# Performance work log

Hardware: AMD Instinct MI355X
Metric: run time of the kernel (lower is better)

## Reference

```python
import jax, jax.numpy as jnp
import numpy as np

DIM = 512
CODEBOOK_SIZE = 8192


def setup_inputs() -> dict:
    key = jax.random.key(0)
    k_x, k_e = jax.random.split(key)
    x = jax.random.normal(k_x, (4, 4096, DIM), dtype=jnp.float32)
    # EuclideanCodebook buffer: embed ~ randn(codebook_size, dim)
    embed = jax.random.normal(k_e, (CODEBOOK_SIZE, DIM), dtype=jnp.float32)
    return {"x": x, "embed": embed}


def reference(x, embed):
    # projection_in / projection_out are Identity (codebook_dim=None)
    shape = x.shape
    flatten = x.reshape(-1, shape[-1])  # [N, D]
    # dist = -(||f||^2 - 2 f @ e^T + ||e||^2)  -> negative squared euclidean
    f_sq = jnp.sum(flatten * flatten, axis=1, keepdims=True)          # [N, 1]
    e_sq = jnp.sum(embed * embed, axis=1)[None, :]                    # [1, K]
    dist = -(f_sq - 2.0 * flatten @ embed.T + e_sq)                   # [N, K]
    embed_ind = jnp.argmax(dist, axis=-1)                             # [N]
    embed_ind = embed_ind.reshape(shape[:-1])                         # [B, S]
    quantize = jnp.take(embed, embed_ind, axis=0)                     # [B, S, D]
    return quantize, embed_ind
```

## Files before the change

kernel.cpp:

```cpp
#include <hip/hip_runtime.h>

#define DIM    512
#define KCODES 8192
#define NROWS  16384
#define NEG_INF -3.402823466e38f
#define MARGIN 1.0f
#define CPR 128

typedef unsigned short ushort_t;
typedef unsigned int uint_t;
typedef __attribute__((ext_vector_type(8))) short v8s;
typedef __attribute__((ext_vector_type(4))) float v4f;

__device__ inline ushort_t f32_to_bf16_rne(float f) {
    uint_t u = __float_as_uint(f);
    uint_t r = u + 0x7fffu + ((u >> 16) & 1u);
    return (ushort_t)(r >> 16);
}

__device__ inline int4 cvt8hi(float4 a, float4 b) {
    ushort_t h[8] = { f32_to_bf16_rne(a.x), f32_to_bf16_rne(a.y),
                      f32_to_bf16_rne(a.z), f32_to_bf16_rne(a.w),
                      f32_to_bf16_rne(b.x), f32_to_bf16_rne(b.y),
                      f32_to_bf16_rne(b.z), f32_to_bf16_rne(b.w) };
    int4 p;
    p.x = (int)((uint_t)h[0] | ((uint_t)h[1] << 16));
    p.y = (int)((uint_t)h[2] | ((uint_t)h[3] << 16));
    p.z = (int)((uint_t)h[4] | ((uint_t)h[5] << 16));
    p.w = (int)((uint_t)h[6] | ((uint_t)h[7] << 16));
    return p;
}

__device__ inline void dma16(const void* g, void* l) {
    __builtin_amdgcn_global_load_lds(
        (const __attribute__((address_space(1))) unsigned int*)g,
        (__attribute__((address_space(3))) unsigned int*)l, 16, 0, 0);
}

__global__ __launch_bounds__(256) void convert_kernel(
    const float* __restrict__ x, const float* __restrict__ embed,
    int4* __restrict__ e_t, int4* __restrict__ x_t,
    float* __restrict__ e_sq, float* __restrict__ esqh,
    float* __restrict__ f_sq)
{
    __shared__ int4 buf[64][65];

    const int w = threadIdx.x >> 6;
    const int lane = threadIdx.x & 63;
    const bool isE = blockIdx.x < (KCODES / 64);
    const int rows0 = isE ? blockIdx.x * 64 : (blockIdx.x - KCODES / 64) * 64;
    const float* src_base = isE ? embed : x;

    #pragma unroll
    for (int rr = 0; rr < 16; ++rr) {
        int r_local = w * 16 + rr;
        const float* src = src_base + (size_t)(rows0 + r_local) * DIM + lane * 8;
        float4 a = *(const float4*)src;
        float4 b = *(const float4*)(src + 4);
        buf[r_local][(lane + 2 * r_local) & 63] = cvt8hi(a, b);
        float s = a.x*a.x + a.y*a.y + a.z*a.z + a.w*a.w
                + b.x*b.x + b.y*b.y + b.z*b.z + b.w*b.w;
        #pragma unroll
        for (int off = 32; off >= 1; off >>= 1) s += __shfl_down(s, off, 64);
        if (lane == 0) {
            int r = rows0 + r_local;
            if (isE) { e_sq[r] = s; esqh[r] = -0.5f * s; }
            else     { f_sq[r] = s; }
        }
    }
    __syncthreads();

    #pragma unroll
    for (int i = 0; i < 16; ++i) {
        int sq = w * 16 + i;
        int4 v = buf[lane][(sq + 2 * lane) & 63];
        if (isE) e_t[(size_t)sq * KCODES + rows0 + lane] = v;
        else     x_t[(size_t)sq * NROWS  + rows0 + lane] = v;
    }
}

__global__ __launch_bounds__(512, 2) void screen_kernel(
    const int4* __restrict__ e_t, const int4* __restrict__ x_t,
    const float* __restrict__ esqh,
    float* __restrict__ cand_s, int* __restrict__ cand_i)
{
    __shared__ __align__(16) short EH[2][8][256][8];
    __shared__ __align__(16) short XH[2][8][256][8];

    const int t = threadIdx.x;
    const int w = t >> 6;
    const int lane = t & 63;
    const int quad = lane >> 4;
    const int l15 = lane & 15;
    const int wm = w & 1;
    const int wn = w >> 1;

    const int n = blockIdx.x;
    const int xcd = n & 7;
    const int j = n >> 3;
    const int rt = xcd * 8 + (j & 7);
    const int ct = j >> 3;
    const int row0 = rt * 256;
    const int cbase = ct * 256;

    const bool isE = w < 4;
    const int4* gbase = isE ? (e_t + cbase + w * 64 + lane)
                            : (x_t + row0 + (w - 4) * 64 + lane);
    const size_t gstride = isE ? KCODES : NROWS;

    v4f acc[8][4];
    #pragma unroll
    for (int mi = 0; mi < 8; ++mi) {
        float4 sd = *(const float4*)(esqh + cbase + wm * 128 + mi * 16 + quad * 4);
        v4f sv = (v4f){sd.x, sd.y, sd.z, sd.w};
        #pragma unroll
        for (int nj = 0; nj < 4; ++nj) acc[mi][nj] = sv;
    }

    auto issue_dma = [&](int S) {
        int buf = S & 1;
        short* ldst = isE ? &EH[buf][0][(w & 3) * 64][0] : &XH[buf][0][(w & 3) * 64][0];
        #pragma unroll
        for (int q = 0; q < 8; ++q) {
            int sq = S * 8 + q;
            dma16(gbase + (size_t)sq * gstride, ldst + q * 256 * 8);
        }
    };

    issue_dma(0);

    for (int S = 0; S < 8; ++S) {
        __syncthreads();
        if (S < 7) issue_dma(S + 1);
        const int buf = S & 1;

        #pragma unroll
        for (int ks = 0; ks < 2; ++ks) {
            const int q = ks * 4 + quad;
            v8s bh[4];
            #pragma unroll
            for (int nj = 0; nj < 4; ++nj)
                bh[nj] = *(const v8s*)(&XH[buf][q][wn * 64 + nj * 16 + l15][0]);
            #pragma unroll
            for (int mi = 0; mi < 8; ++mi) {
                v8s ah = *(const v8s*)(&EH[buf][q][wm * 128 + mi * 16 + l15][0]);
                #pragma unroll
                for (int nj = 0; nj < 4; ++nj)
                    acc[mi][nj] = __builtin_amdgcn_mfma_f32_16x16x32_bf16(ah, bh[nj], acc[mi][nj], 0, 0, 0);
            }
        }
    }

    #pragma unroll
    for (int nj = 0; nj < 4; ++nj) {
        float b1 = NEG_INF, b2 = NEG_INF;
        int   i1 = 0, i2 = 0;
        #pragma unroll
        for (int g = 0; g < 4; ++g) {
            v4f s0 = acc[2 * g][nj], s1 = acc[2 * g + 1][nj];
            float m = fmaxf(fmaxf(fmaxf(s0[0], s0[1]), fmaxf(s0[2], s0[3])),
                            fmaxf(fmaxf(s1[0], s1[1]), fmaxf(s1[2], s1[3])));
            int gid = cbase + wm * 128 + g * 32 + quad * 4;
            if (m > b1)      { b2 = b1; i2 = i1; b1 = m; i1 = gid; }
            else if (m > b2) { b2 = m;  i2 = gid; }
        }
        #pragma unroll
        for (int o = 16; o <= 32; o <<= 1) {
            float c1 = __shfl_xor(b1, o, 64);
            int   j1 = __shfl_xor(i1, o, 64);
            float c2 = __shfl_xor(b2, o, 64);
            int   j2 = __shfl_xor(i2, o, 64);
            if (c1 > b1) {
                b2 = fmaxf(b1, c2); i2 = (b1 >= c2) ? i1 : j2;
                b1 = c1; i1 = j1;
            } else {
                i2 = (b2 >= c1) ? i2 : j1;
                b2 = fmaxf(b2, c1);
            }
        }
        if (quad == 0) {
            int row = row0 + wn * 64 + nj * 16 + l15;
            size_t b = (size_t)row * CPR + (ct * 4 + wm * 2);
            cand_s[b]     = b1;  cand_i[b]     = i1;
            cand_s[b + 1] = b2;  cand_i[b + 1] = i2;
        }
    }
}

__global__ __launch_bounds__(256) void rescore_kernel(
    const float* __restrict__ x, const float* __restrict__ embed,
    const float* __restrict__ e_sq, const float* __restrict__ f_sq,
    const float* __restrict__ cand_s, const int* __restrict__ cand_i,
    float* __restrict__ out)
{
    int row = blockIdx.x * 4 + (threadIdx.x >> 6);
    int lane = threadIdx.x & 63;
    size_t cb = (size_t)row * CPR;

    float cs0 = cand_s[cb + lane];
    float cs1 = cand_s[cb + 64 + lane];
    int   ci0 = cand_i[cb + lane];
    int   ci1 = cand_i[cb + 64 + lane];

    float m = fmaxf(cs0, cs1);
    #pragma unroll
    for (int o = 32; o >= 1; o >>= 1) m = fmaxf(m, __shfl_xor(m, o, 64));

    unsigned long long mask0 = __ballot(cs0 >= m - MARGIN);
    unsigned long long mask1 = __ballot(cs1 >= m - MARGIN);

    const float4* xsrc = (const float4*)(x + (size_t)row * DIM + lane * 8);
    float4 xa = xsrc[0], xb = xsrc[1];
    float fsq = f_sq[row];

    float bd = NEG_INF;
    int   bi = 0x7fffffff;

    #pragma unroll
    for (int s = 0; s < 2; ++s) {
        unsigned long long mask = s ? mask1 : mask0;
        while (mask) {
            int p = __ffsll(mask) - 1;
            mask &= mask - 1;
            int base = __shfl(s ? ci1 : ci0, p);
            #pragma unroll
            for (int e8 = 0; e8 < 8; ++e8) {
                int c = base + ((e8 >> 2) << 4) + (e8 & 3);
                const float4* er = (const float4*)(embed + (size_t)c * DIM + lane * 8);
                float4 ea = er[0], eb = er[1];
                float part = xa.x*ea.x + xa.y*ea.y + xa.z*ea.z + xa.w*ea.w
                           + xb.x*eb.x + xb.y*eb.y + xb.z*eb.z + xb.w*eb.w;
                #pragma unroll
                for (int o = 32; o >= 1; o >>= 1) part += __shfl_xor(part, o, 64);
                float d = -((fsq - 2.0f * part) + e_sq[c]);
                if (d > bd || (d == bd && c < bi)) { bd = d; bi = c; }
            }
        }
    }

    const float4* er = (const float4*)(embed + (size_t)bi * DIM + lane * 8);
    float4 qa = er[0], qb = er[1];
    float4* dst = (float4*)(out + (size_t)row * DIM + lane * 8);
    dst[0] = qa; dst[1] = qb;
    if (lane == 0) out[(size_t)NROWS * DIM + row] = (float)bi;
}

extern "C" void kernel_launch(void* const* d_in, const int* in_sizes, int n_in,
                              void* d_out, int out_size, void* d_ws, size_t ws_size,
                              hipStream_t stream)
{
    const float* x     = (const float*)d_in[0];
    const float* embed = (const float*)d_in[1];
    float* out = (float*)d_out;

    float* e_sq   = (float*)d_ws;
    float* esqh   = e_sq + KCODES;
    float* f_sq   = esqh + KCODES;
    float* cand_s = f_sq + NROWS;
    int*   cand_i = (int*)(cand_s + (size_t)NROWS * CPR);
    int4*  e_t    = (int4*)(cand_i + (size_t)NROWS * CPR);

    int4* x_t = (int4*)d_out;

    (void)in_sizes; (void)n_in; (void)out_size; (void)ws_size;

    convert_kernel<<<(KCODES + NROWS) / 64, 256, 0, stream>>>(
        x, embed, e_t, x_t, e_sq, esqh, f_sq);
    screen_kernel<<<2048, 512, 0, stream>>>(
        e_t, x_t, esqh, cand_s, cand_i);
    rescore_kernel<<<NROWS / 4, 256, 0, stream>>>(
        x, embed, e_sq, f_sq, cand_s, cand_i, out);
}
```

Baseline: 268.6 us.

## Interleave global-to-LDS DMA with MFMA phases using fine-grained waitcnt and setprio

Restructures the main K-loop into four phases, each loading half the A/B fragments from LDS and then running 16 MFMAs. The prefetch DMA for the next stage is spread across the phases two chunks at a time. Explicit vmcnt/lgkmcnt waits and raw s_barrier calls replace the single __syncthreads per stage, and s_setprio raises wave priority around the MFMA bursts. The goal is to hide global-load and LDS latency behind matrix work and to cut synchronization stalls. In exchange it adds more barriers and relies on hand-counted waitcnt values, which is a correctness risk.

New measurement: 271.6 us. No clear change (+1.1%).

```diff
diff --git a/kernel.cpp b/kernel.cpp
--- a/kernel.cpp
+++ b/kernel.cpp
@@ -117,38 +117,91 @@
         for (int nj = 0; nj < 4; ++nj) acc[mi][nj] = sv;
     }
 
-    auto issue_dma = [&](int S) {
+    auto issue_q = [&](int S, int q) {
         int buf = S & 1;
-        short* ldst = isE ? &EH[buf][0][(w & 3) * 64][0] : &XH[buf][0][(w & 3) * 64][0];
-        #pragma unroll
-        for (int q = 0; q < 8; ++q) {
-            int sq = S * 8 + q;
-            dma16(gbase + (size_t)sq * gstride, ldst + q * 256 * 8);
-        }
+        short* ldst = isE ? &EH[buf][q][(w & 3) * 64][0]
+                          : &XH[buf][q][(w & 3) * 64][0];
+        dma16(gbase + (size_t)(S * 8 + q) * gstride, ldst);
     };
 
-    issue_dma(0);
+    #pragma unroll
+    for (int q = 0; q < 8; ++q) issue_q(0, q);
+    asm volatile("s_waitcnt vmcnt(4)" ::: "memory");
+    __builtin_amdgcn_s_barrier();
 
     for (int S = 0; S < 8; ++S) {
-        __syncthreads();
-        if (S < 7) issue_dma(S + 1);
         const int buf = S & 1;
-
-        #pragma unroll
-        for (int ks = 0; ks < 2; ++ks) {
-            const int q = ks * 4 + quad;
-            v8s bh[4];
+        const bool pf = (S < 7);
+        v8s bh[4], ah[4];
+
+        #pragma unroll
+        for (int nj = 0; nj < 4; ++nj)
+            bh[nj] = *(const v8s*)(&XH[buf][quad][wn * 64 + nj * 16 + l15][0]);
+        #pragma unroll
+        for (int mi = 0; mi < 4; ++mi)
+            ah[mi] = *(const v8s*)(&EH[buf][quad][wm * 128 + mi * 16 + l15][0]);
+        if (pf) { issue_q(S + 1, 0); issue_q(S + 1, 1); }
+        __builtin_amdgcn_s_barrier();
+        asm volatile("s_waitcnt lgkmcnt(0)" ::: "memory");
+        __builtin_amdgcn_s_setprio(1);
+        #pragma unroll
+        for (int mi = 0; mi < 4; ++mi)
             #pragma unroll
             for (int nj = 0; nj < 4; ++nj)
-                bh[nj] = *(const v8s*)(&XH[buf][q][wn * 64 + nj * 16 + l15][0]);
-            #pragma unroll
-            for (int mi = 0; mi < 8; ++mi) {
-                v8s ah = *(const v8s*)(&EH[buf][q][wm * 128 + mi * 16 + l15][0]);
-                #pragma unroll
-                for (int nj = 0; nj < 4; ++nj)
-                    acc[mi][nj] = __builtin_amdgcn_mfma_f32_16x16x32_bf16(ah, bh[nj], acc[mi][nj], 0, 0, 0);
-            }
-        }
+                acc[mi][nj] = __builtin_amdgcn_mfma_f32_16x16x32_bf16(ah[mi], bh[nj], acc[mi][nj], 0, 0, 0);
+        __builtin_amdgcn_s_setprio(0);
+        __builtin_amdgcn_s_barrier();
+
+        #pragma unroll
+        for (int mi = 0; mi < 4; ++mi)
+            ah[mi] = *(const v8s*)(&EH[buf][quad][wm * 128 + (4 + mi) * 16 + l15][0]);
+        if (pf) { issue_q(S + 1, 2); issue_q(S + 1, 3); }
+        __builtin_amdgcn_s_barrier();
+        asm volatile("s_waitcnt lgkmcnt(0)" ::: "memory");
+        __builtin_amdgcn_s_setprio(1);
+        #pragma unroll
+        for (int mi = 0; mi < 4; ++mi)
+            #pragma unroll
+            for (int nj = 0; nj < 4; ++nj)
+                acc[4 + mi][nj] = __builtin_amdgcn_mfma_f32_16x16x32_bf16(ah[mi], bh[nj], acc[4 + mi][nj], 0, 0, 0);
+        __builtin_amdgcn_s_setprio(0);
+        if (pf) asm volatile("s_waitcnt vmcnt(4)" ::: "memory");
+        else    asm volatile("s_waitcnt vmcnt(0)" ::: "memory");
+        __builtin_amdgcn_s_barrier();
+
+        #pragma unroll
+        for (int nj = 0; nj < 4; ++nj)
+            bh[nj] = *(const v8s*)(&XH[buf][4 + quad][wn * 64 + nj * 16 + l15][0]);
+        #pragma unroll
+        for (int mi = 0; mi < 4; ++mi)
+            ah[mi] = *(const v8s*)(&EH[buf][4 + quad][wm * 128 + mi * 16 + l15][0]);
+        if (pf) { issue_q(S + 1, 4); issue_q(S + 1, 5); }
+        __builtin_amdgcn_s_barrier();
+        asm volatile("s_waitcnt lgkmcnt(0)" ::: "memory");
+        __builtin_amdgcn_s_setprio(1);
+        #pragma unroll
+        for (int mi = 0; mi < 4; ++mi)
+            #pragma unroll
+            for (int nj = 0; nj < 4; ++nj)
+                acc[mi][nj] = __builtin_amdgcn_mfma_f32_16x16x32_bf16(ah[mi], bh[nj], acc[mi][nj], 0, 0, 0);
+        __builtin_amdgcn_s_setprio(0);
+        __builtin_amdgcn_s_barrier();
+
+        #pragma unroll
+        for (int mi = 0; mi < 4; ++mi)
+            ah[mi] = *(const v8s*)(&EH[buf][4 + quad][wm * 128 + (4 + mi) * 16 + l15][0]);
+        if (pf) { issue_q(S + 1, 6); issue_q(S + 1, 7); }
+        __builtin_amdgcn_s_barrier();
+        asm volatile("s_waitcnt lgkmcnt(0)" ::: "memory");
+        __builtin_amdgcn_s_setprio(1);
+        #pragma unroll
+        for (int mi = 0; mi < 4; ++mi)
+            #pragma unroll
+            for (int nj = 0; nj < 4; ++nj)
+                acc[4 + mi][nj] = __builtin_amdgcn_mfma_f32_16x16x32_bf16(ah[mi], bh[nj], acc[4 + mi][nj], 0, 0, 0);
+        __builtin_amdgcn_s_setprio(0);
+        if (pf) asm volatile("s_waitcnt vmcnt(4)" ::: "memory");
+        __builtin_amdgcn_s_barrier();
     }
 
     #pragma unroll
```

## Load codebook fragments directly from global into registers, stage only X in LDS

Applied to the files above, without the earlier changes.

The codebook operand (A) of the screening GEMM is no longer staged through shared memory. Each wave now loads its A fragments straight from global memory into registers, double-buffered and prefetched one k-step ahead. Only the X tile stays in LDS, and all 8 waves share its DMA. This halves LDS footprint and LDS read traffic, but makes A loads redundant across the four waves with the same wm and adds register pressure plus exposed global-load latency.

New measurement: 298.9 us. 1.11x slower.

```diff
diff --git a/kernel.cpp b/kernel.cpp
--- a/kernel.cpp
+++ b/kernel.cpp
@@ -84,7 +84,6 @@
     const float* __restrict__ esqh,
     float* __restrict__ cand_s, int* __restrict__ cand_i)
 {
-    __shared__ __align__(16) short EH[2][8][256][8];
     __shared__ __align__(16) short XH[2][8][256][8];
 
     const int t = threadIdx.x;
@@ -103,10 +102,8 @@
     const int row0 = rt * 256;
     const int cbase = ct * 256;
 
-    const bool isE = w < 4;
-    const int4* gbase = isE ? (e_t + cbase + w * 64 + lane)
-                            : (x_t + row0 + (w - 4) * 64 + lane);
-    const size_t gstride = isE ? KCODES : NROWS;
+    const int4* xg = x_t + row0 + lane;
+    const int4* ag = e_t + cbase + wm * 128 + l15;
 
     v4f acc[8][4];
     #pragma unroll
@@ -117,38 +114,50 @@
         for (int nj = 0; nj < 4; ++nj) acc[mi][nj] = sv;
     }
 
-    auto issue_dma = [&](int S) {
+    auto stageX = [&](int S) {
         int buf = S & 1;
-        short* ldst = isE ? &EH[buf][0][(w & 3) * 64][0] : &XH[buf][0][(w & 3) * 64][0];
-        #pragma unroll
-        for (int q = 0; q < 8; ++q) {
-            int sq = S * 8 + q;
-            dma16(gbase + (size_t)sq * gstride, ldst + q * 256 * 8);
-        }
+        size_t sq = (size_t)(S * 8 + w);
+        short* dst = &XH[buf][w][0][0];
+        #pragma unroll
+        for (int i = 0; i < 4; ++i)
+            dma16(xg + sq * NROWS + i * 64, dst + i * 64 * 8);
     };
 
-    issue_dma(0);
+    v8s afA[8], afB[8];
+    auto loadA = [&](v8s (&af)[8], int sq) {
+        #pragma unroll
+        for (int mi = 0; mi < 8; ++mi)
+            af[mi] = *(const v8s*)(ag + (size_t)sq * KCODES + mi * 16);
+    };
+
+    stageX(0);
+    loadA(afA, quad);
 
     for (int S = 0; S < 8; ++S) {
         __syncthreads();
-        if (S < 7) issue_dma(S + 1);
+        if (S < 7) stageX(S + 1);
         const int buf = S & 1;
-
-        #pragma unroll
-        for (int ks = 0; ks < 2; ++ks) {
-            const int q = ks * 4 + quad;
-            v8s bh[4];
+        v8s bh[4];
+
+        #pragma unroll
+        for (int nj = 0; nj < 4; ++nj)
+            bh[nj] = *(const v8s*)(&XH[buf][quad][wn * 64 + nj * 16 + l15][0]);
+        loadA(afB, S * 8 + 4 + quad);
+        #pragma unroll
+        for (int mi = 0; mi < 8; ++mi)
             #pragma unroll
             for (int nj = 0; nj < 4; ++nj)
-                bh[nj] = *(const v8s*)(&XH[buf][q][wn * 64 + nj * 16 + l15][0]);
+                acc[mi][nj] = __builtin_amdgcn_mfma_f32_16x16x32_bf16(afA[mi], bh[nj], acc[mi][nj], 0, 0, 0);
+
+        #pragma unroll
+        for (int nj = 0; nj < 4; ++nj)
+            bh[nj] = *(const v8s*)(&XH[buf][4 + quad][wn * 64 + nj * 16 + l15][0]);
+        if (S < 7) loadA(afA, (S + 1) * 8 + quad);
+        #pragma unroll
+        for (int mi = 0; mi < 8; ++mi)
             #pragma unroll
-            for (int mi = 0; mi < 8; ++mi) {
-                v8s ah = *(const v8s*)(&EH[buf][q][wm * 128 + mi * 16 + l15][0]);
-                #pragma unroll
-                for (int nj = 0; nj < 4; ++nj)
-                    acc[mi][nj] = __builtin_amdgcn_mfma_f32_16x16x32_bf16(ah, bh[nj], acc[mi][nj], 0, 0, 0);
-            }
-        }
+            for (int nj = 0; nj < 4; ++nj)
+                acc[mi][nj] = __builtin_amdgcn_mfma_f32_16x16x32_bf16(afB[mi], bh[nj], acc[mi][nj], 0, 0, 0);
     }
 
     #pragma unroll
```
